# Kernel optimization log

Measured on AMD Instinct MI355X. Metric: run time of the kernel, lower is better.

Reference implementation:

```python
import jax, jax.numpy as jnp
from jax import lax
import numpy as np

B, H, W = 8, 1024, 1024
NUM_POINTS = 10
THRESHOLD_RATIO = 0.5
K_PEAKS = 512  # cap on peak candidates fed to greedy NMS


def setup_inputs() -> dict:
    key = jax.random.key(0)
    ks = jax.random.split(key, 8)
    return {
        "rgb_image": jax.random.uniform(ks[0], (B, 3, H, W), jnp.float32),
        "depth_image": jax.random.uniform(ks[1], (B, 1, H, W), jnp.float32),
        "conv1_w": jax.random.normal(ks[2], (32, 12, 3, 3), jnp.float32) * 0.1,
        "conv1_b": jax.random.normal(ks[3], (32,), jnp.float32) * 0.1,
        "bn_gamma": jnp.ones((32,), jnp.float32),
        "bn_beta": jnp.zeros((32,), jnp.float32),
        "bn_mean": jax.random.normal(ks[4], (32,), jnp.float32) * 0.1,
        "bn_var": jax.random.uniform(ks[5], (32,), jnp.float32) + 0.5,
        "conv2_w": jax.random.normal(ks[6], (1, 32, 1, 1), jnp.float32) * 0.1,
        "conv2_b": jnp.zeros((1,), jnp.float32),
    }


def dwt2(x):
    # Haar DWT exactly as in the torch module (row split then column split)
    x01 = x[..., 0::2, :] * 0.5
    x02 = x[..., 1::2, :] * 0.5
    LL = x01[..., 0::2] + x02[..., 0::2]
    LH = x01[..., 0::2] - x02[..., 0::2]
    HL = x01[..., 1::2] + x02[..., 1::2]
    HH = x01[..., 1::2] - x02[..., 1::2]
    return LL, LH, HL, HH


def conv2d(x, w, b=None, pad=0, groups=1):
    y = lax.conv_general_dilated(x, w, (1, 1), [(pad, pad), (pad, pad)],
                                 dimension_numbers=("NCHW", "OIHW", "NCHW"),
                                 feature_group_count=groups)
    if b is not None:
        y = y + b[None, :, None, None]
    return y


def gaussian_smooth(x, k=5, sigma=1.0):
    ax = jnp.arange(-(k // 2), k // 2 + 1, dtype=jnp.float32)
    xx, yy = jnp.meshgrid(ax, ax, indexing="ij")
    ker = jnp.exp(-(xx ** 2 + yy ** 2) / (2.0 * sigma ** 2))
    ker = ker / ker.sum()
    C = x.shape[1]
    wk = jnp.tile(ker[None, None], (C, 1, 1, 1))  # depthwise
    return conv2d(x, wk, pad=k // 2, groups=C)


def find_points(s):
    """Greedy spatial-NMS peak picking on a single (h,w) saliency map.
    Returns (NUM_POINTS, 2) normalized (x, y) coords."""
    h, w = s.shape
    min_dist = float(max(max(h, w) // 20, 20))
    flat = s.reshape(-1)
    mp = lax.reduce_window(s, -jnp.inf, lax.max, (3, 3), (1, 1), [(1, 1), (1, 1)])
    peak_flat = ((s == mp) & (s > 0)).reshape(-1)
    peak_scores = jnp.where(peak_flat, flat, -jnp.inf)
    top_vals, top_idx = lax.top_k(peak_scores, K_PEAKS)  # sorted desc = torch argsort
    valid = top_vals > -jnp.inf
    px = (top_idx % w).astype(jnp.float32)
    py = (top_idx // w).astype(jnp.float32)
    pc = jnp.stack([px, py], axis=-1)                     # (K,2)
    dist = jnp.sqrt(((pc[:, None, :] - pc[None, :, :]) ** 2).sum(-1))  # (K,K)
    ar = jnp.arange(K_PEAKS)

    def body(i, st):
        avail, sel, cnt = st
        take = avail[i] & valid[i] & (cnt < NUM_POINTS)
        sel = sel.at[i].set(take)
        suppress = (dist[i] < min_dist) & (ar > i)  # nearby[:i+1]=False in torch
        avail = jnp.where(take, avail & (~suppress), avail)
        return avail, sel, cnt + take.astype(jnp.int32)

    _, sel, n_chosen = lax.fori_loop(
        0, K_PEAKS, body,
        (jnp.ones(K_PEAKS, bool), jnp.zeros(K_PEAKS, bool), jnp.int32(0)))

    # compact chosen peak indices (in descending-score order) into first slots
    pos = jnp.cumsum(sel.astype(jnp.int32)) - 1
    scatter_pos = jnp.where(sel, pos, NUM_POINTS)  # out-of-range -> dropped
    buf = jnp.zeros(NUM_POINTS, jnp.int32).at[scatter_pos].set(top_idx, mode="drop")
    # fallback: top saliency excluding all peaks (matches torch fill-up branch)
    fb_scores = jnp.where(peak_flat, -jnp.inf, flat)
    _, fb_idx = lax.top_k(fb_scores, NUM_POINTS)
    slot = jnp.arange(NUM_POINTS)
    fb = fb_idx[jnp.clip(slot - n_chosen, 0, NUM_POINTS - 1)]
    sel_idx = jnp.where(slot < n_chosen, buf, fb)
    cx = (sel_idx % w).astype(jnp.float32) / w
    cy = (sel_idx // w).astype(jnp.float32) / h
    return jnp.stack([cx, cy], axis=-1)


def boxes_from_mask(masks):
    binm = masks[:, 0] > THRESHOLD_RATIO  # (B,H,W)
    Hh, Ww = binm.shape[1], binm.shape[2]
    rows = binm.any(axis=2)
    cols = binm.any(axis=1)
    ri = jnp.arange(Hh)
    ci = jnp.arange(Ww)
    rmin = jnp.min(jnp.where(rows, ri[None, :], Hh), axis=1)
    rmax = jnp.max(jnp.where(rows, ri[None, :], -1), axis=1)
    cmin = jnp.min(jnp.where(cols, ci[None, :], Ww), axis=1)
    cmax = jnp.max(jnp.where(cols, ci[None, :], -1), axis=1)
    has = rows.any(axis=1)
    boxes = jnp.stack([cmin, rmin, cmax, rmax], axis=-1).astype(jnp.float32)
    default = jnp.array([0.0, 0.0, Ww - 1.0, Hh - 1.0], jnp.float32)
    return jnp.where(has[:, None], boxes, default[None, :])


def reference(rgb_image, depth_image, conv1_w, conv1_b, bn_gamma, bn_beta,
              bn_mean, bn_var, conv2_w, conv2_b):
    rgb_gray = rgb_image.mean(axis=1, keepdims=True)
    rLL, rLH, rHL, rHH = dwt2(rgb_gray)
    dLL, dLH, dHL, dHH = dwt2(depth_image)
    E_rgb = jnp.sqrt(rLH ** 2 + rHL ** 2 + rHH ** 2 + 1e-8)
    E_depth = jnp.sqrt(dLH ** 2 + dHL ** 2 + dHH ** 2 + 1e-8)
    E_rgb_s = gaussian_smooth(E_rgb)
    E_depth_s = gaussian_smooth(E_depth)
    freq = jnp.concatenate(
        [rLL, rLH, rHL, rHH, dLL, dLH, dHL, dHH, E_rgb, E_depth, E_rgb_s, E_depth_s],
        axis=1)  # (B,12,H/2,W/2)
    x = conv2d(freq, conv1_w, conv1_b, pad=1)
    inv = lax.rsqrt(bn_var + 1e-5)
    x = bn_gamma[None, :, None, None] * (x - bn_mean[None, :, None, None]) * inv[None, :, None, None] + bn_beta[None, :, None, None]
    x = jax.nn.gelu(x)
    sal = jax.nn.sigmoid(conv2d(x, conv2_w, conv2_b))  # (B,1,H/2,W/2)
    masks = jax.image.resize(sal, (sal.shape[0], 1, H, W), method="bilinear")
    coords = jax.vmap(find_points)(sal[:, 0])          # (B,N,2)
    labels = jnp.ones((sal.shape[0], NUM_POINTS), jnp.int32)
    boxes = boxes_from_mask(masks)                     # (B,4)
    return coords, labels, boxes, masks
```

## Files before the change

kernel.cpp:

```cpp
#include <hip/hip_runtime.h>
#include <math.h>


#define CHW 262144
#define FULLHW 1048576
#define NB1 64
#define NB2 32
#define PROW 514
#define PREC (514*514)
#define LREC 130

typedef __attribute__((ext_vector_type(8))) short bf16x8;
typedef __attribute__((ext_vector_type(16))) float f32x16;

static __device__ __forceinline__ unsigned short f2bf(float x) {
  unsigned u = __float_as_uint(x);
  u += 0x7FFFu + ((u >> 16) & 1u);
  return (unsigned short)(u >> 16);
}
static __device__ __forceinline__ float bf2f(unsigned short h) {
  return __uint_as_float(((unsigned)h) << 16);
}

static constexpr size_t OFF_SAL   = 0;
static constexpr size_t OFF_THR   = 8388608;
static constexpr size_t OFF_CNT   = OFF_THR + 256;
static constexpr size_t OFF_CAND  = OFF_CNT + 256;
static constexpr size_t OFF_PART  = OFF_CAND + 131072;
static constexpr size_t OFF_APACK = OFF_PART + 32768;
static constexpr size_t OFF_EP    = OFF_APACK + 20480;
static constexpr size_t OFF_PKM   = OFF_EP + 512;
static constexpr size_t OFF_DYN   = OFF_PKM + 2097152;

static constexpr int SDY[9] = {-1,-1,-1, 0,0,0, 1,1,1};
static constexpr int SDX[9] = {-1, 0, 1,-1,0,1,-1,0,1};

__global__ void k_init(unsigned* __restrict__ cnt,
                       const float* __restrict__ w1, const float* __restrict__ b1,
                       const float* __restrict__ gam, const float* __restrict__ bet,
                       const float* __restrict__ mean, const float* __restrict__ var,
                       const float* __restrict__ w2, const float* __restrict__ b2,
                       unsigned short* __restrict__ apack, float* __restrict__ ep) {
  int i = blockIdx.x * 256 + threadIdx.x;
  if (i < 16) cnt[i] = 0;
  if (i < 9216) {
    int e = i & 7, lane = (i >> 3) & 63, frag = i >> 9;
    int s = frag >> 1, hh = frag & 1;
    int co = lane & 31;
    int c = ((lane >> 5) << 3) + e;
    float val = (c < 12) ? w1[co * 108 + c * 9 + s] : 0.0f;
    unsigned short hb = f2bf(val);
    apack[i] = hh ? f2bf(val - bf2f(hb)) : hb;
  }
  if (i < 96) {
    int t = i >> 5, rem = i & 31, kg = rem >> 4, reg = rem & 15;
    int co = (reg & 3) + 8 * (reg >> 2) + 4 * kg;
    float sc = gam[co] * rsqrtf(var[co] + 1e-5f);
    float v = (t == 0) ? sc
            : (t == 1) ? (b1[co] - mean[co]) * sc + bet[co]
                       : w2[co];
    ep[i] = v;
  } else if (i == 96) {
    ep[96] = b2[0];
  }
}

__global__ __launch_bounds__(256) void k_zero(unsigned short* __restrict__ freq2) {
  int i = blockIdx.x * 256 + threadIdx.x;
  int bi = blockIdx.y;
  if (i >= 8208) return;
  int pl = i / 2052, r = i % 2052;
  int row, col;
  if (r < 514)        { row = 0;   col = r; }
  else if (r < 1028)  { row = 513; col = r - 514; }
  else if (r < 1540)  { row = r - 1028 + 1; col = 0; }
  else                { row = r - 1540 + 1; col = 513; }
  uint4* p = (uint4*)(freq2 + ((size_t)(bi * 4 + pl) * PREC + (size_t)row * PROW + col) * 8);
  *p = make_uint4(0u, 0u, 0u, 0u);
}

__global__ __launch_bounds__(256) void k_freq(const float* __restrict__ rgb,
                                              const float* __restrict__ dep,
                                              unsigned short* __restrict__ freq2,
                                              float* __restrict__ ebuf, int b0) {
  int t = blockIdx.x * 256 + threadIdx.x;
  int bi = blockIdx.y;
  int b = b0 + bi;
  int xp = t & 255, y = t >> 8;
  const float* base = rgb + (size_t)b * 3 * FULLHW + (size_t)(2 * y) * 1024 + 4 * xp;
  float4 R0 = *(const float4*)(base);
  float4 R1 = *(const float4*)(base + 1024);
  float4 G0 = *(const float4*)(base + FULLHW);
  float4 G1 = *(const float4*)(base + FULLHW + 1024);
  float4 Bl0 = *(const float4*)(base + 2 * FULLHW);
  float4 Bl1 = *(const float4*)(base + 2 * FULLHW + 1024);
  const float* dbase = dep + (size_t)b * FULLHW + (size_t)(2 * y) * 1024 + 4 * xp;
  float4 D0 = *(const float4*)(dbase);
  float4 D1 = *(const float4*)(dbase + 1024);

  float gt[4], gb[4], dt[4], db_[4];
  gt[0] = (R0.x + G0.x + Bl0.x) / 3.0f; gt[1] = (R0.y + G0.y + Bl0.y) / 3.0f;
  gt[2] = (R0.z + G0.z + Bl0.z) / 3.0f; gt[3] = (R0.w + G0.w + Bl0.w) / 3.0f;
  gb[0] = (R1.x + G1.x + Bl1.x) / 3.0f; gb[1] = (R1.y + G1.y + Bl1.y) / 3.0f;
  gb[2] = (R1.z + G1.z + Bl1.z) / 3.0f; gb[3] = (R1.w + G1.w + Bl1.w) / 3.0f;
  dt[0] = D0.x; dt[1] = D0.y; dt[2] = D0.z; dt[3] = D0.w;
  db_[0] = D1.x; db_[1] = D1.y; db_[2] = D1.z; db_[3] = D1.w;

  unsigned short hs[2][8], ls[2][8];
  float er[2], ed[2];
  #pragma unroll
  for (int j = 0; j < 2; ++j) {
    float a = gt[2 * j] * 0.5f, bb = gb[2 * j] * 0.5f;
    float c = gt[2 * j + 1] * 0.5f, d = gb[2 * j + 1] * 0.5f;
    float v[8];
    v[0] = a + bb; v[1] = a - bb; v[2] = c + d; v[3] = c - d;
    float da = dt[2 * j] * 0.5f, db2 = db_[2 * j] * 0.5f;
    float dc = dt[2 * j + 1] * 0.5f, dd = db_[2 * j + 1] * 0.5f;
    v[4] = da + db2; v[5] = da - db2; v[6] = dc + dd; v[7] = dc - dd;
    er[j] = sqrtf(v[1] * v[1] + v[2] * v[2] + v[3] * v[3] + 1e-8f);
    ed[j] = sqrtf(v[5] * v[5] + v[6] * v[6] + v[7] * v[7] + 1e-8f);
    #pragma unroll
    for (int cc = 0; cc < 8; ++cc) {
      unsigned short hb = f2bf(v[cc]);
      hs[j][cc] = hb;
      ls[j][cc] = f2bf(v[cc] - bf2f(hb));
    }
  }
  size_t rbase = (size_t)(y + 1) * PROW + (2 * xp + 1);
  unsigned short* d0 = freq2 + ((size_t)(bi * 4 + 0) * PREC + rbase) * 8;
  unsigned short* d1 = freq2 + ((size_t)(bi * 4 + 1) * PREC + rbase) * 8;
  ((uint4*)d0)[0] = ((const uint4*)hs[0])[0];
  ((uint4*)d0)[1] = ((const uint4*)hs[1])[0];
  ((uint4*)d1)[0] = ((const uint4*)ls[0])[0];
  ((uint4*)d1)[1] = ((const uint4*)ls[1])[0];
  float* eb = ebuf + (size_t)bi * 2 * CHW + (size_t)y * 512 + 2 * xp;
  *(float2*)(eb) = make_float2(er[0], er[1]);
  *(float2*)(eb + CHW) = make_float2(ed[0], ed[1]);
}

__constant__ float GW[25] = {
  0.00296901f, 0.01330621f, 0.02193824f, 0.01330621f, 0.00296901f,
  0.01330621f, 0.05963435f, 0.09832035f, 0.05963435f, 0.01330621f,
  0.02193824f, 0.09832035f, 0.16210276f, 0.09832035f, 0.02193824f,
  0.01330621f, 0.05963435f, 0.09832035f, 0.05963435f, 0.01330621f,
  0.00296901f, 0.01330621f, 0.02193824f, 0.01330621f, 0.00296901f};

__global__ __launch_bounds__(256) void k_smooth(const float* __restrict__ ebuf,
                                                unsigned short* __restrict__ freq2) {
  int t = blockIdx.x * 256 + threadIdx.x;
  int bi = blockIdx.y;
  int x = t & 511, y = t >> 9;
  const float* eb = ebuf + (size_t)bi * 2 * CHW;
  float accv[2];
  #pragma unroll
  for (int ch = 0; ch < 2; ++ch) {
    const float* fin = eb + ch * CHW;
    float acc = 0.0f;
    #pragma unroll
    for (int i = 0; i < 5; ++i) {
      int yy = y + i - 2;
      if (yy < 0 || yy > 511) continue;
      #pragma unroll
      for (int j = 0; j < 5; ++j) {
        int xx = x + j - 2;
        if (xx < 0 || xx > 511) continue;
        acc += GW[i * 5 + j] * fin[yy * 512 + xx];
      }
    }
    accv[ch] = acc;
  }
  float erc = eb[t], edc = eb[CHW + t];
  unsigned short rh[8], rl[8];
  float v4[4] = {erc, edc, accv[0], accv[1]};
  #pragma unroll
  for (int j = 0; j < 4; ++j) {
    unsigned short hb = f2bf(v4[j]);
    rh[j] = hb;
    rl[j] = f2bf(v4[j] - bf2f(hb));
  }
  #pragma unroll
  for (int j = 4; j < 8; ++j) { rh[j] = 0; rl[j] = 0; }
  size_t rbase = (size_t)(y + 1) * PROW + (x + 1);
  unsigned short* p2 = freq2 + ((size_t)(bi * 4 + 2) * PREC + rbase) * 8;
  unsigned short* p3 = freq2 + ((size_t)(bi * 4 + 3) * PREC + rbase) * 8;
  *(uint4*)p2 = *(const uint4*)rh;
  *(uint4*)p3 = *(const uint4*)rl;
}

__global__ __launch_bounds__(256) void k_conv(const unsigned short* __restrict__ freq2,
    const unsigned short* __restrict__ apack, const float* __restrict__ ep,
    float* __restrict__ sal, int b0) {
  __shared__ __align__(16) char smem[24960];
  int tid = threadIdx.x;
  int l = tid & 63, wv = tid >> 6;
  int y = blockIdx.y;
  int xwb = blockIdx.x * 128;
  int bi = blockIdx.z;
  int n = l & 31, kg = l >> 5;

  #pragma unroll
  for (int it = 0; it < 7; ++it) {
    int j = it * 256 + tid;
    if (j < 1560) {
      int row = j / 520, rem = j % 520;
      int plane = rem / 130, rec = rem % 130;
      const unsigned short* g = freq2 +
          ((size_t)(bi * 4 + plane) * PREC + (size_t)(y + row) * PROW + (xwb + rec)) * 8;
      *(uint4*)(smem + j * 16) = *(const uint4*)g;
    }
  }
  __syncthreads();

  const unsigned short* ab = apack + l * 8;
  f32x16 acc = {};
  #pragma unroll
  for (int s = 0; s < 9; ++s) {
    int row = 1 + SDY[s];
    int rec = wv * 32 + n + 1 + SDX[s];
    const char* bh = smem + (((row * 4 + kg * 2 + 0) * LREC) + rec) * 16;
    const char* bl = smem + (((row * 4 + kg * 2 + 1) * LREC) + rec) * 16;
    bf16x8 Bh = *(const bf16x8*)bh;
    bf16x8 Bl = *(const bf16x8*)bl;
    bf16x8 Ah = *(const bf16x8*)(ab + s * 1024);
    bf16x8 Al = *(const bf16x8*)(ab + s * 1024 + 512);
    acc = __builtin_amdgcn_mfma_f32_32x32x16_bf16(Ah, Bh, acc, 0, 0, 0);
    acc = __builtin_amdgcn_mfma_f32_32x32x16_bf16(Al, Bh, acc, 0, 0, 0);
    acc = __builtin_amdgcn_mfma_f32_32x32x16_bf16(Ah, Bl, acc, 0, 0, 0);
  }

  const float* e0 = ep + kg * 16;
  const float* e1 = ep + 32 + kg * 16;
  const float* e2 = ep + 64 + kg * 16;
  float s2 = 0.0f;
  #pragma unroll
  for (int r = 0; r < 16; ++r) {
    float t = acc[r] * e0[r] + e1[r];
    float z = t * (1.5957691216057308f + 0.07135481283247183f * (t * t));
    float g = t * __builtin_amdgcn_rcpf(1.0f + __expf(-z));
    s2 += g * e2[r];
  }
  s2 += __shfl_xor(s2, 32);
  s2 += ep[96];
  float res = __builtin_amdgcn_rcpf(1.0f + __expf(-s2));
  if (l < 32)
    sal[(size_t)(b0 + bi) * CHW + (size_t)y * 512 + xwb + wv * 32 + n] = res;
}

__global__ __launch_bounds__(256) void k_resize(const float* __restrict__ sal,
                                                float* __restrict__ masks,
                                                int* __restrict__ part) {
  int b = blockIdx.y;
  int blk = blockIdx.x;
  int t = threadIdx.x;
  const float* sp = sal + (size_t)b * CHW;
  float* mp = masks + (size_t)b * FULLHW;
  int mnX = 0x7FFFFFFF, mxX = -1, mnY = 0x7FFFFFFF, mxY = -1;
  int c0 = 4 * t;
  #pragma unroll
  for (int r = 0; r < 4; ++r) {
    int Y = blk * 4 + r;
    int y0 = (Y - 1) >> 1;
    float wy = (Y & 1) ? 0.25f : 0.75f;
    int y0c = y0 < 0 ? 0 : y0, y1c = (y0 + 1 > 511) ? 511 : y0 + 1;
    const float* r0 = sp + y0c * 512;
    const float* r1 = sp + y1c * 512;
    float o[4];
    #pragma unroll
    for (int j = 0; j < 4; ++j) {
      int X = c0 + j;
      int x0 = (X - 1) >> 1;
      float wx = (X & 1) ? 0.25f : 0.75f;
      int x0c = x0 < 0 ? 0 : x0, x1c = (x0 + 1 > 511) ? 511 : x0 + 1;
      float v00 = r0[x0c], v01 = r0[x1c], v10 = r1[x0c], v11 = r1[x1c];
      o[j] = (1.0f - wy) * ((1.0f - wx) * v00 + wx * v01)
           + wy * ((1.0f - wx) * v10 + wx * v11);
      if (o[j] > 0.5f) {
        mnX = min(mnX, X); mxX = max(mxX, X);
        mnY = min(mnY, Y); mxY = max(mxY, Y);
      }
    }
    *(float4*)(mp + (size_t)Y * 1024 + c0) = make_float4(o[0], o[1], o[2], o[3]);
  }
  __shared__ int s0[256], s1[256], s2[256], s3[256];
  s0[t] = mnX; s1[t] = mxX; s2[t] = mnY; s3[t] = mxY;
  __syncthreads();
  for (int off = 128; off > 0; off >>= 1) {
    if (t < off) {
      s0[t] = min(s0[t], s0[t + off]); s1[t] = max(s1[t], s1[t + off]);
      s2[t] = min(s2[t], s2[t + off]); s3[t] = max(s3[t], s3[t + off]);
    }
    __syncthreads();
  }
  if (t == 0) {
    int* pp = part + (b * 256 + blk) * 4;
    pp[0] = s0[0]; pp[1] = s1[0]; pp[2] = s2[0]; pp[3] = s3[0];
  }
}

__global__ __launch_bounds__(256) void k_boxreduce(const int* __restrict__ part,
                                                   float* __restrict__ out) {
  int b = blockIdx.x, t = threadIdx.x;
  const int* pp = part + (b * 256 + t) * 4;
  __shared__ int s0[256], s1[256], s2[256], s3[256];
  s0[t] = pp[0]; s1[t] = pp[1]; s2[t] = pp[2]; s3[t] = pp[3];
  __syncthreads();
  for (int off = 128; off > 0; off >>= 1) {
    if (t < off) {
      s0[t] = min(s0[t], s0[t + off]); s1[t] = max(s1[t], s1[t + off]);
      s2[t] = min(s2[t], s2[t + off]); s3[t] = max(s3[t], s3[t + off]);
    }
    __syncthreads();
  }
  if (t == 0) {
    float x0, y0, x1, y1;
    if (s3[0] < 0) { x0 = 0.0f; y0 = 0.0f; x1 = 1023.0f; y1 = 1023.0f; }
    else { x0 = (float)s0[0]; y0 = (float)s2[0]; x1 = (float)s1[0]; y1 = (float)s3[0]; }
    out[240 + b * 4 + 0] = x0;
    out[240 + b * 4 + 1] = y0;
    out[240 + b * 4 + 2] = x1;
    out[240 + b * 4 + 3] = y1;
  }
}

__global__ __launch_bounds__(256) void k_hist1(const float* __restrict__ sal,
                                               unsigned* __restrict__ h1p,
                                               unsigned char* __restrict__ pkm) {
  __shared__ unsigned sH[4096];
  int b = blockIdx.y, tid = threadIdx.x;
  for (int i = tid; i < 4096; i += 256) sH[i] = 0;
  __syncthreads();
  const float* sp = sal + (size_t)b * CHW;
  int base = blockIdx.x * 4096;
  for (int it = 0; it < 4; ++it) {
    int p = base + it * 1024 + tid * 4;
    int x0 = p & 511, y = p >> 9;
    int ym = (y > 0) ? y - 1 : 0, yp = (y < 511) ? y + 1 : 511;
    const float* r0 = sp + ym * 512;
    const float* r1 = sp + y * 512;
    const float* r2 = sp + yp * 512;
    float4 m0 = *(const float4*)(r0 + x0);
    float4 m1 = *(const float4*)(r1 + x0);
    float4 m2 = *(const float4*)(r2 + x0);
    float l0 = x0 ? r0[x0 - 1] : m0.x;
    float l1 = x0 ? r1[x0 - 1] : m1.x;
    float l2 = x0 ? r2[x0 - 1] : m2.x;
    float q0 = (x0 < 508) ? r0[x0 + 4] : m0.w;
    float q1 = (x0 < 508) ? r1[x0 + 4] : m1.w;
    float q2 = (x0 < 508) ? r2[x0 + 4] : m2.w;
    float a0[6] = {l0, m0.x, m0.y, m0.z, m0.w, q0};
    float a1[6] = {l1, m1.x, m1.y, m1.z, m1.w, q1};
    float a2[6] = {l2, m2.x, m2.y, m2.z, m2.w, q2};
    unsigned pw = 0;
    #pragma unroll
    for (int j = 0; j < 4; ++j) {
      float r0m = fmaxf(fmaxf(a0[j], a0[j + 1]), a0[j + 2]);
      float r1m = fmaxf(fmaxf(a1[j], a1[j + 1]), a1[j + 2]);
      float r2m = fmaxf(fmaxf(a2[j], a2[j + 1]), a2[j + 2]);
      float cmax = fmaxf(fmaxf(r0m, r1m), r2m);
      float sv = a1[j + 1];
      bool pk = (sv > 0.0f) && (sv >= cmax);
      pw |= (pk ? 1u : 0u) << (8 * j);
      unsigned bin = (__float_as_uint(sv) >> 21) & 2047;
      atomicAdd(&sH[(pk ? 0 : 2048) + bin], 1u);
    }
    *(unsigned*)(pkm + (size_t)b * CHW + p) = pw;
  }
  __syncthreads();
  unsigned* dst = h1p + ((size_t)b * NB1 + blockIdx.x) * 4096;
  for (int i = tid; i < 4096; i += 256) dst[i] = sH[i];
}

__global__ __launch_bounds__(256) void k_scan(const unsigned* __restrict__ hp,
                                              int* __restrict__ thr, int level,
                                              int np) {
  int c = blockIdx.x, b = blockIdx.y, t = threadIdx.x;
  __shared__ unsigned sBins[2048];
  __shared__ unsigned sS[256];
  __shared__ int sT;
  unsigned bv[8] = {0, 0, 0, 0, 0, 0, 0, 0};
  for (int p = 0; p < np; ++p) {
    const unsigned* q = hp + ((size_t)(b * np + p)) * 4096 + c * 2048 + t * 8;
    uint4 a = *(const uint4*)(q);
    uint4 d = *(const uint4*)(q + 4);
    bv[0] += a.x; bv[1] += a.y; bv[2] += a.z; bv[3] += a.w;
    bv[4] += d.x; bv[5] += d.y; bv[6] += d.z; bv[7] += d.w;
  }
  unsigned part = 0;
  #pragma unroll
  for (int r = 0; r < 8; ++r) {
    sBins[t * 8 + r] = bv[r];
    part += bv[r];
  }
  sS[t] = part;
  __syncthreads();
  for (int off = 1; off < 256; off <<= 1) {
    unsigned add = (t + off < 256) ? sS[t + off] : 0;
    __syncthreads();
    sS[t] += add;
    __syncthreads();
  }
  int K = (c == 0) ? 512 : 10;
  int* tb = thr + (c * 8 + b) * 4;
  if (level == 1) { K -= tb[1]; if (K < 1) K = 1; }
  if (t == 0) sT = -1;
  __syncthreads();
  if (sS[t] >= (unsigned)K && (t == 255 || sS[t + 1] < (unsigned)K)) sT = t;
  __syncthreads();
  if (t == 0) {
    int T = 0;
    unsigned run = 0;
    if (sT >= 0) {
      int ts = sT;
      run = (ts < 255) ? sS[ts + 1] : 0;
      for (int r = 7; r >= 0; --r) {
        unsigned v = sBins[ts * 8 + r];
        run += v;
        if (run >= (unsigned)K) { T = ts * 8 + r; run -= v; break; }
      }
    } else {
      T = 0;
      run = sS[0] - sBins[0];
    }
    if (level == 0) { tb[0] = T; tb[1] = (int)run; }
    else           { tb[2] = (tb[0] << 11) | T; }
  }
}

__global__ __launch_bounds__(256) void k_hist2(const float* __restrict__ sal,
                                               const unsigned char* __restrict__ pkm,
                                               const int* __restrict__ thr,
                                               unsigned* __restrict__ h2p) {
  __shared__ unsigned sH[4096];
  int b = blockIdx.y, tid = threadIdx.x;
  for (int i = tid; i < 4096; i += 256) sH[i] = 0;
  __syncthreads();
  int t0 = thr[(0 * 8 + b) * 4];
  int t1 = thr[(1 * 8 + b) * 4];
  const float* sp = sal + (size_t)b * CHW;
  const unsigned char* pp = pkm + (size_t)b * CHW;
  int base = blockIdx.x * 8192;
  for (int it = 0; it < 8; ++it) {
    int p = base + it * 1024 + tid * 4;
    float4 s4 = *(const float4*)(sp + p);
    unsigned pk4 = *(const unsigned*)(pp + p);
    float sv[4] = {s4.x, s4.y, s4.z, s4.w};
    #pragma unroll
    for (int j = 0; j < 4; ++j) {
      bool pk = ((pk4 >> (8 * j)) & 255u) != 0;
      unsigned bits = __float_as_uint(sv[j]);
      int tt = pk ? t0 : t1;
      if ((int)(bits >> 21) == tt)
        atomicAdd(&sH[(pk ? 0 : 2048) + ((bits >> 10) & 2047)], 1u);
    }
  }
  __syncthreads();
  unsigned* dst = h2p + ((size_t)b * NB2 + blockIdx.x) * 4096;
  for (int i = tid; i < 4096; i += 256) dst[i] = sH[i];
}

__global__ __launch_bounds__(256) void k_compact(const float* __restrict__ sal,
                                                 const unsigned char* __restrict__ pkm,
                                                 const int* __restrict__ thr,
                                                 unsigned* __restrict__ cnt,
                                                 unsigned long long* __restrict__ cand) {
  int b = blockIdx.y;
  int p = (blockIdx.x * 256 + threadIdx.x) * 4;
  const float* sp = sal + (size_t)b * CHW;
  float4 s4 = *(const float4*)(sp + p);
  unsigned pk4 = *(const unsigned*)(pkm + (size_t)b * CHW + p);
  unsigned q0 = (unsigned)thr[(0 * 8 + b) * 4 + 2];
  unsigned q1 = (unsigned)thr[(1 * 8 + b) * 4 + 2];
  float sv[4] = {s4.x, s4.y, s4.z, s4.w};
  #pragma unroll
  for (int j = 0; j < 4; ++j) {
    bool pk = ((pk4 >> (8 * j)) & 255u) != 0;
    unsigned bits = __float_as_uint(sv[j]);
    unsigned q = pk ? q0 : q1;
    int c = pk ? 0 : 1;
    if ((bits >> 10) >= q) {
      unsigned pos = atomicAdd(&cnt[c * 8 + b], 1u);
      if (pos < 1024)
        cand[((size_t)(c * 8 + b) << 10) + pos] =
            ((unsigned long long)bits << 32) | (unsigned)(~(p + j));
    }
  }
}

__device__ inline void bitonic1024_desc(unsigned long long* sKey) {
  int t = threadIdx.x;
  for (unsigned k = 2; k <= 1024; k <<= 1) {
    for (unsigned j = k >> 1; j > 0; j >>= 1) {
      __syncthreads();
      #pragma unroll
      for (int e = 0; e < 2; ++e) {
        unsigned i = (unsigned)t + (unsigned)e * 512u;
        unsigned l = i ^ j;
        if (l > i) {
          unsigned long long a = sKey[i], bb = sKey[l];
          if (((i & k) == 0) ? (a < bb) : (a > bb)) { sKey[i] = bb; sKey[l] = a; }
        }
      }
    }
  }
  __syncthreads();
}

__global__ __launch_bounds__(512) void k_nms(const unsigned long long* __restrict__ cand,
                                             const unsigned* __restrict__ cnt,
                                             float* __restrict__ out) {
  __shared__ unsigned long long sKey[1024];
  __shared__ unsigned sIdx[512];
  __shared__ int sAvail[512];
  __shared__ int sSel[16];
  int b = blockIdx.x, t = threadIdx.x;
  if (t < 10) out[160 + b * 10 + t] = 1.0f;
  int Cp = (int)cnt[b]; if (Cp > 1024) Cp = 1024;
  const unsigned long long* cp = cand + ((size_t)b << 10);
  sKey[t] = (t < Cp) ? cp[t] : 0ULL;
  sKey[t + 512] = (t + 512 < Cp) ? cp[t + 512] : 0ULL;
  bitonic1024_desc(sKey);
  sIdx[t] = (unsigned)(~sKey[t]);
  int ncand = (Cp < 512) ? Cp : 512;
  sAvail[t] = (t < ncand) ? 1 : 0;
  __syncthreads();
  int nsel = 0;
  for (int i = 0; i < 512 && nsel < 10; ++i) {
    if (sAvail[i] != 0) {
      unsigned pi = sIdx[i];
      int xi = (int)(pi & 511), yi = (int)(pi >> 9);
      if (t > i && sAvail[t]) {
        int dx = (int)(sIdx[t] & 511) - xi;
        int dy = (int)(sIdx[t] >> 9) - yi;
        if (dx * dx + dy * dy < 625) sAvail[t] = 0;
      }
      if (t == 0) sSel[nsel] = (int)pi;
      ++nsel;
      __syncthreads();
    }
  }
  __syncthreads();
  int Cf = (int)cnt[8 + b]; if (Cf > 1024) Cf = 1024;
  const unsigned long long* cf = cand + ((size_t)(8 + b) << 10);
  sKey[t] = (t < Cf) ? cf[t] : 0ULL;
  sKey[t + 512] = (t + 512 < Cf) ? cf[t + 512] : 0ULL;
  bitonic1024_desc(sKey);
  if (t < 10) {
    int fi;
    if (t < nsel) fi = sSel[t];
    else { int r = t - nsel; if (r > 9) r = 9; fi = (int)((unsigned)(~sKey[r])); }
    out[((size_t)b * 10 + t) * 2 + 0] = (float)(fi & 511) * (1.0f / 512.0f);
    out[((size_t)b * 10 + t) * 2 + 1] = (float)(fi >> 9) * (1.0f / 512.0f);
  }
}

extern "C" void kernel_launch(void* const* d_in, const int* in_sizes, int n_in,
                              void* d_out, int out_size, void* d_ws, size_t ws_size,
                              hipStream_t stream) {
  const float* rgb  = (const float*)d_in[0];
  const float* dep  = (const float*)d_in[1];
  const float* w1   = (const float*)d_in[2];
  const float* b1   = (const float*)d_in[3];
  const float* gam  = (const float*)d_in[4];
  const float* bet  = (const float*)d_in[5];
  const float* bmn  = (const float*)d_in[6];
  const float* bvr  = (const float*)d_in[7];
  const float* w2   = (const float*)d_in[8];
  const float* b2   = (const float*)d_in[9];
  float* out = (float*)d_out;
  char* ws = (char*)d_ws;

  float* sal = (float*)(ws + OFF_SAL);
  int* thr = (int*)(ws + OFF_THR);
  unsigned* cnt = (unsigned*)(ws + OFF_CNT);
  unsigned long long* cand = (unsigned long long*)(ws + OFF_CAND);
  int* part = (int*)(ws + OFF_PART);
  unsigned short* apack = (unsigned short*)(ws + OFF_APACK);
  float* ep = (float*)(ws + OFF_EP);
  unsigned char* pkm = (unsigned char*)(ws + OFF_PKM);

  size_t perE = (size_t)2 * CHW * 4;
  size_t perF = (size_t)PREC * 64;
  long long avail = (long long)ws_size - (long long)OFF_DYN;
  int nb = 1;
  if (avail >= (long long)(perE + perF)) {
    long long m = avail / (long long)(perE + perF);
    nb = (m > 8) ? 8 : (int)m;
  }
  float* ebuf = (float*)(ws + OFF_DYN);
  unsigned short* freq2 = (unsigned short*)(ws + OFF_DYN + perE * (size_t)nb);
  unsigned* h1p = (unsigned*)(ws + OFF_DYN);
  unsigned* h2p = (unsigned*)(ws + OFF_DYN + (size_t)8 * NB1 * 4096 * 4);

  k_init<<<40, 256, 0, stream>>>(cnt, w1, b1, gam, bet, bmn, bvr, w2, b2,
                                 apack, ep);
  k_zero<<<dim3(33, nb), 256, 0, stream>>>(freq2);

  for (int b0 = 0; b0 < 8; b0 += nb) {
    int nbc = (8 - b0 < nb) ? (8 - b0) : nb;
    k_freq<<<dim3(512, nbc), 256, 0, stream>>>(rgb, dep, freq2, ebuf, b0);
    k_smooth<<<dim3(1024, nbc), 256, 0, stream>>>(ebuf, freq2);
    k_conv<<<dim3(4, 512, nbc), 256, 0, stream>>>(freq2, apack, ep, sal, b0);
  }

  k_resize<<<dim3(256, 8), 256, 0, stream>>>(sal, out + 272, part);
  k_boxreduce<<<8, 256, 0, stream>>>(part, out);
  k_hist1<<<dim3(NB1, 8), 256, 0, stream>>>(sal, h1p, pkm);
  k_scan<<<dim3(2, 8), 256, 0, stream>>>(h1p, thr, 0, NB1);
  k_hist2<<<dim3(NB2, 8), 256, 0, stream>>>(sal, pkm, thr, h2p);
  k_scan<<<dim3(2, 8), 256, 0, stream>>>(h2p, thr, 1, NB2);
  k_compact<<<dim3(256, 8), 256, 0, stream>>>(sal, pkm, thr, cnt, cand);
  k_nms<<<8, 512, 0, stream>>>(cand, cnt, out);
}
```

Measured before the change: 509.8 us.

## Compute four output rows per conv block to reuse halo rows and weights

```diff
diff --git a/kernel.cpp b/kernel.cpp
--- a/kernel.cpp
+++ b/kernel.cpp
@@ -190,60 +190,71 @@
 __global__ __launch_bounds__(256) void k_conv(const unsigned short* __restrict__ freq2,
     const unsigned short* __restrict__ apack, const float* __restrict__ ep,
     float* __restrict__ sal, int b0) {
-  __shared__ __align__(16) char smem[24960];
+  __shared__ __align__(16) char smem[49920];
   int tid = threadIdx.x;
   int l = tid & 63, wv = tid >> 6;
-  int y = blockIdx.y;
+  int yb = blockIdx.y * 4;
   int xwb = blockIdx.x * 128;
   int bi = blockIdx.z;
   int n = l & 31, kg = l >> 5;
 
   #pragma unroll
-  for (int it = 0; it < 7; ++it) {
+  for (int it = 0; it < 13; ++it) {
     int j = it * 256 + tid;
-    if (j < 1560) {
-      int row = j / 520, rem = j % 520;
-      int plane = rem / 130, rec = rem % 130;
+    if (j < 3120) {
+      int row = j / 520, rem = j - row * 520;
+      int plane = rem / 130, rec = rem - plane * 130;
       const unsigned short* g = freq2 +
-          ((size_t)(bi * 4 + plane) * PREC + (size_t)(y + row) * PROW + (xwb + rec)) * 8;
+          ((size_t)(bi * 4 + plane) * PREC + (size_t)(yb + row) * PROW + (xwb + rec)) * 8;
       *(uint4*)(smem + j * 16) = *(const uint4*)g;
     }
   }
-  __syncthreads();
 
   const unsigned short* ab = apack + l * 8;
-  f32x16 acc = {};
+  bf16x8 Ah[9], Al[9];
   #pragma unroll
   for (int s = 0; s < 9; ++s) {
-    int row = 1 + SDY[s];
-    int rec = wv * 32 + n + 1 + SDX[s];
-    const char* bh = smem + (((row * 4 + kg * 2 + 0) * LREC) + rec) * 16;
-    const char* bl = smem + (((row * 4 + kg * 2 + 1) * LREC) + rec) * 16;
-    bf16x8 Bh = *(const bf16x8*)bh;
-    bf16x8 Bl = *(const bf16x8*)bl;
-    bf16x8 Ah = *(const bf16x8*)(ab + s * 1024);
-    bf16x8 Al = *(const bf16x8*)(ab + s * 1024 + 512);
-    acc = __builtin_amdgcn_mfma_f32_32x32x16_bf16(Ah, Bh, acc, 0, 0, 0);
-    acc = __builtin_amdgcn_mfma_f32_32x32x16_bf16(Al, Bh, acc, 0, 0, 0);
-    acc = __builtin_amdgcn_mfma_f32_32x32x16_bf16(Ah, Bl, acc, 0, 0, 0);
+    Ah[s] = *(const bf16x8*)(ab + s * 1024);
+    Al[s] = *(const bf16x8*)(ab + s * 1024 + 512);
   }
 
   const float* e0 = ep + kg * 16;
   const float* e1 = ep + 32 + kg * 16;
   const float* e2 = ep + 64 + kg * 16;
-  float s2 = 0.0f;
-  #pragma unroll
-  for (int r = 0; r < 16; ++r) {
-    float t = acc[r] * e0[r] + e1[r];
-    float z = t * (1.5957691216057308f + 0.07135481283247183f * (t * t));
-    float g = t * __builtin_amdgcn_rcpf(1.0f + __expf(-z));
-    s2 += g * e2[r];
-  }
-  s2 += __shfl_xor(s2, 32);
-  s2 += ep[96];
-  float res = __builtin_amdgcn_rcpf(1.0f + __expf(-s2));
-  if (l < 32)
-    sal[(size_t)(b0 + bi) * CHW + (size_t)y * 512 + xwb + wv * 32 + n] = res;
+  float b2v = ep[96];
+
+  __syncthreads();
+
+  #pragma unroll
+  for (int ry = 0; ry < 4; ++ry) {
+    f32x16 acc = {};
+    #pragma unroll
+    for (int s = 0; s < 9; ++s) {
+      int row = ry + 1 + SDY[s];
+      int rec = wv * 32 + n + 1 + SDX[s];
+      const char* bh = smem + (((row * 4 + kg * 2 + 0) * LREC) + rec) * 16;
+      const char* bl = smem + (((row * 4 + kg * 2 + 1) * LREC) + rec) * 16;
+      bf16x8 Bh = *(const bf16x8*)bh;
+      bf16x8 Bl = *(const bf16x8*)bl;
+      acc = __builtin_amdgcn_mfma_f32_32x32x16_bf16(Ah[s], Bh, acc, 0, 0, 0);
+      acc = __builtin_amdgcn_mfma_f32_32x32x16_bf16(Al[s], Bh, acc, 0, 0, 0);
+      acc = __builtin_amdgcn_mfma_f32_32x32x16_bf16(Ah[s], Bl, acc, 0, 0, 0);
+    }
+
+    float s2 = 0.0f;
+    #pragma unroll
+    for (int r = 0; r < 16; ++r) {
+      float t = acc[r] * e0[r] + e1[r];
+      float z = t * (1.5957691216057308f + 0.07135481283247183f * (t * t));
+      float g = t * __builtin_amdgcn_rcpf(1.0f + __expf(-z));
+      s2 += g * e2[r];
+    }
+    s2 += __shfl_xor(s2, 32);
+    s2 += b2v;
+    float res = __builtin_amdgcn_rcpf(1.0f + __expf(-s2));
+    if (l < 32)
+      sal[(size_t)(b0 + bi) * CHW + (size_t)(yb + ry) * 512 + xwb + wv * 32 + n] = res;
+  }
 }
 
 __global__ __launch_bounds__(256) void k_resize(const float* __restrict__ sal,
@@ -599,7 +610,7 @@
     int nbc = (8 - b0 < nb) ? (8 - b0) : nb;
     k_freq<<<dim3(512, nbc), 256, 0, stream>>>(rgb, dep, freq2, ebuf, b0);
     k_smooth<<<dim3(1024, nbc), 256, 0, stream>>>(ebuf, freq2);
-    k_conv<<<dim3(4, 512, nbc), 256, 0, stream>>>(freq2, apack, ep, sal, b0);
+    k_conv<<<dim3(4, 128, nbc), 256, 0, stream>>>(freq2, apack, ep, sal, b0);
   }
 
   k_resize<<<dim3(256, 8), 256, 0, stream>>>(sal, out + 272, part);
```

Result: no change. 505.1 us (-0.9%).
